# Optimization experiments

Hardware: AMD Instinct MI355X
Metric: run time of the kernel (lower is better)

Reference implementation:

```python
import jax, jax.numpy as jnp
import numpy as np
from jax import lax

DIM = 256
KS = 7
EPS = 1e-6


def setup_inputs() -> dict:
    key = jax.random.key(0)
    ks = jax.random.split(key, 10)
    x = jax.random.normal(ks[0], (32, DIM, 56, 56), dtype=jnp.float32)
    mask = jax.random.randint(ks[1], (32, 1, 7, 7), 0, 2, dtype=jnp.int32)
    dw_w = jax.random.normal(ks[2], (DIM, 1, KS, KS), dtype=jnp.float32) * (1.0 / KS)
    dw_b = jax.random.normal(ks[3], (DIM,), dtype=jnp.float32) * 0.01
    ln_w = jnp.ones((DIM,), dtype=jnp.float32)
    ln_b = jnp.zeros((DIM,), dtype=jnp.float32)
    w1 = jax.random.normal(ks[4], (DIM, 4 * DIM), dtype=jnp.float32) * (1.0 / np.sqrt(DIM))
    b1 = jax.random.normal(ks[5], (4 * DIM,), dtype=jnp.float32) * 0.01
    w2 = jax.random.normal(ks[6], (4 * DIM, DIM), dtype=jnp.float32) * (1.0 / np.sqrt(4 * DIM))
    b2 = jax.random.normal(ks[7], (DIM,), dtype=jnp.float32) * 0.01
    gamma = jnp.full((DIM,), 1e-6, dtype=jnp.float32)
    return {"x": x, "mask": mask, "dw_w": dw_w, "dw_b": dw_b, "ln_w": ln_w,
            "ln_b": ln_b, "w1": w1, "b1": b1, "w2": w2, "b2": b2, "gamma": gamma}


def _expand_mask(mask, H, W):
    # repeat_interleave the (B,1,f,f) mask up to (B,1,H,W)
    hr, wr = H // mask.shape[-2], W // mask.shape[-1]
    m = jnp.repeat(jnp.repeat(mask, hr, axis=2), wr, axis=3)
    return m


def reference(x, mask, dw_w, dw_b, ln_w, ln_b, w1, b1, w2, b2, gamma):
    B, C, H, W = x.shape
    m = _expand_mask(mask, H, W).astype(x.dtype)  # (B,1,H,W)
    inp = x
    # depthwise conv, 'same' padding
    pad = KS // 2
    y = lax.conv_general_dilated(
        x, dw_w, window_strides=(1, 1), padding=[(pad, pad), (pad, pad)],
        feature_group_count=C, dimension_numbers=("NCHW", "OIHW", "NCHW"))
    y = y + dw_b[None, :, None, None]
    y = y.transpose(0, 2, 3, 1)  # (B,H,W,C)
    # sparse LayerNorm: gather-norm-scatter == per-position LN zeroed at inactive
    mu = jnp.mean(y, axis=-1, keepdims=True)
    var = jnp.mean((y - mu) ** 2, axis=-1, keepdims=True)
    y = ((y - mu) * lax.rsqrt(var + EPS)) * ln_w + ln_b
    y = y * m[:, 0, :, :, None]
    # MLP
    h = jax.nn.gelu(jnp.einsum("bhwc,cd->bhwd", y, w1) + b1, approximate=False)
    z = (jnp.einsum("bhwd,dc->bhwc", h, w2) + b2) * gamma
    z = z.transpose(0, 3, 1, 2)  # (B,C,H,W)
    z = z * m
    return inp + z
```

## Files before the change

### kernel.cpp

```cpp
#include <hip/hip_runtime.h>
#include <math.h>

#define HW   56
#define DIMC 256
#define HID  1024

typedef __attribute__((ext_vector_type(8))) short bf16x8;
typedef __attribute__((ext_vector_type(4))) float f32x4;

__device__ __forceinline__ short f2bf(float f) {
  union { float fv; unsigned u; } v; v.fv = f;
  unsigned r = v.u + 0x7fffu + ((v.u >> 16) & 1u);
  return (short)(r >> 16);
}
__device__ __forceinline__ float bf2f(short s) {
  union { unsigned u; float fv; } v; v.u = ((unsigned)(unsigned short)s) << 16;
  return v.fv;
}
__device__ __forceinline__ float gelu_fast(float v) {
  float e = exp2f(-2.4556260f * v);
  return v * __builtin_amdgcn_rcpf(1.f + e);
}
__device__ __forceinline__ long pk8(float f0, float f1, float f2, float f3,
                                    float f4, float f5, float f6, float f7) {
  int lo = __builtin_amdgcn_cvt_pk_fp8_f32(f0, f1, 0, false);
  lo = __builtin_amdgcn_cvt_pk_fp8_f32(f2, f3, lo, true);
  int hi = __builtin_amdgcn_cvt_pk_fp8_f32(f4, f5, 0, false);
  hi = __builtin_amdgcn_cvt_pk_fp8_f32(f6, f7, hi, true);
  return ((long)(unsigned)lo) | ((long)hi << 32);
}
__device__ __forceinline__ char f2fp8(float f) {
  return (char)(__builtin_amdgcn_cvt_pk_fp8_f32(f, f, 0, false) & 0xff);
}

__global__ void prep_pack(const float* __restrict__ w1, const float* __restrict__ w2,
                          long* __restrict__ w1p, long* __restrict__ w2p,
                          int* __restrict__ qmeta) {
  int g = blockIdx.x * 256 + threadIdx.x;
  if (g == 0) { qmeta[0] = 0; qmeta[1] = 0; qmeta[2] = 0; }
  int f = g >> 6, lane = g & 63;
  int l15 = lane & 15, q = lane >> 4;
  float t[8];
  if (f < 512) {
    int k8 = f & 7, tt = f >> 3, nt = tt & 1, ch = tt >> 1;
    int n = ch * 32 + nt * 16 + l15;
    int k = k8 * 32 + q * 8;
    #pragma unroll
    for (int j = 0; j < 8; ++j) t[j] = w1[(k + j) * HID + n];
    w1p[f * 64 + lane] = pk8(t[0], t[1], t[2], t[3], t[4], t[5], t[6], t[7]);
  } else {
    int f2 = f - 512;
    int nt2 = f2 & 15, ch = f2 >> 4;
    int k = ch * 32 + q * 8;
    int c = nt2 * 16 + l15;
    #pragma unroll
    for (int j = 0; j < 8; ++j) t[j] = w2[(k + j) * DIMC + c];
    w2p[f2 * 64 + lane] = pk8(t[0], t[1], t[2], t[3], t[4], t[5], t[6], t[7]);
  }
}

__global__ void compact_k(const int* __restrict__ mask, int* __restrict__ qmeta) {
  int t = blockIdx.x * 256 + threadIdx.x;
  if (t < 1568 && mask[t]) {
    int i = atomicAdd(qmeta, 1);
    qmeta[16 + i] = t;
  }
}

__global__ __launch_bounds__(256, 4) void conv_k(
    const float* __restrict__ x, const int* __restrict__ mask,
    const float* __restrict__ dw_w, const float* __restrict__ dw_b,
    short* __restrict__ ybuf) {
  __shared__ __align__(16) float s_plane[62 * 64];
  __shared__ __align__(16) short s_out[56 * 64];

  int bid = blockIdx.x;
  int c = bid & 255, b = bid >> 8;
  int tid = threadIdx.x;
  const float* xp = x + (long)(b * DIMC + c) * HW * HW;

  #pragma unroll
  for (int it = 0; it < 4; ++it) {
    int slot = tid + 256 * it;
    if (slot < 992) {
      int row = slot >> 4, jj = slot & 15;
      f32x4 v = (f32x4){0.f, 0.f, 0.f, 0.f};
      if (row >= 3 && row < 59 && jj >= 1 && jj <= 14)
        v = *(const f32x4*)(xp + (row - 3) * HW + (jj * 4 - 4));
      *(f32x4*)(s_plane + row * 64 + jj * 4) = v;
    }
  }

  float wt[49];
  #pragma unroll
  for (int j = 0; j < 49; ++j) {
    int wi = __builtin_amdgcn_readfirstlane(__builtin_bit_cast(int, dw_w[c * 49 + j]));
    wt[j] = __builtin_bit_cast(float, wi);
  }
  float db = dw_b[c];
  __syncthreads();

  int cp = tid & 31, rg = tid >> 5;
  if (cp < 28) {
    int col0 = cp * 2, wb = col0 >> 3;
    int r0 = rg * 7;
    int mrow = 0;
    #pragma unroll
    for (int hb = 0; hb < 7; ++hb)
      mrow |= (mask[(b * 7 + hb) * 7 + wb] ? 1 : 0) << hb;
    int hb1 = r0 >> 3, hb2 = (r0 + 6) >> 3;
    if (mrow & ((2 << hb2) - (1 << hb1))) {
      float W[7][10];
#define LDROW(S, LR) do { int _o = (LR) * 64 + col0;                         \
      W[S][0] = s_plane[_o + 0]; W[S][1] = s_plane[_o + 1];                  \
      W[S][2] = s_plane[_o + 2]; W[S][3] = s_plane[_o + 3];                  \
      W[S][4] = s_plane[_o + 4]; W[S][5] = s_plane[_o + 5];                  \
      W[S][6] = s_plane[_o + 6]; W[S][7] = s_plane[_o + 7];                  \
      W[S][8] = s_plane[_o + 8]; W[S][9] = s_plane[_o + 9]; } while (0)
      LDROW(0, r0 + 0); LDROW(1, r0 + 1); LDROW(2, r0 + 2);
      LDROW(3, r0 + 3); LDROW(4, r0 + 4); LDROW(5, r0 + 5);
      #pragma unroll
      for (int k = 0; k < 7; ++k) {
        LDROW((6 + k) % 7, r0 + 6 + k);
        int r = r0 + k;
        if ((mrow >> (r >> 3)) & 1) {
          float out0 = 0.f, out1 = 0.f;
          #pragma unroll
          for (int dy = 0; dy < 7; ++dy) {
            const float* wr = wt + dy * 7;
            const float* ww = W[(k + dy) % 7];
            #pragma unroll
            for (int dx = 0; dx < 7; ++dx) {
              out0 += wr[dx] * ww[1 + dx];
              out1 += wr[dx] * ww[2 + dx];
            }
          }
          unsigned pk = (unsigned)(unsigned short)f2bf(out0 + db)
                      | ((unsigned)(unsigned short)f2bf(out1 + db) << 16);
          ((int*)s_out)[r * 32 + cp] = (int)pk;
        }
      }
#undef LDROW
    }
  }
  __syncthreads();

  #pragma unroll
  for (int it = 0; it < 2; ++it) {
    int u = tid + 256 * it;
    if (u < 392) {
      int hh = u & 7, th = u >> 3;
      int hbL = th / 7, wbL = th % 7;
      int tile = (b * 7 + hbL) * 7 + wbL;
      if (mask[tile]) {
        bf16x8 v = *(const bf16x8*)(s_out + (hbL * 8 + hh) * 64 + wbL * 8);
        *(bf16x8*)(ybuf + ((long)tile * DIMC + c) * 64 + hh * 8) = v;
      }
    }
  }
}

__global__ __launch_bounds__(256, 3) void mlp_k(
    const float* __restrict__ ln_w, const float* __restrict__ ln_b,
    const float* __restrict__ b1v, const float* __restrict__ b2v,
    const float* __restrict__ gammav,
    const long* __restrict__ w1p, const long* __restrict__ w2p,
    int* __restrict__ qmeta, short* __restrict__ ybuf) {
  __shared__ __align__(16) char smem[46592];
  __shared__ int s_u;
  short* s_a   = (short*)smem;
  short* s_del = (short*)smem;
  char*  s_h8  = smem + 36864;
  float* s_p1  = (float*)(smem + 41984);
  float* s_p2  = (float*)(smem + 43008);
  float* s_mu  = (float*)(smem + 44032);
  float* s_rs  = (float*)(smem + 44288);
  float* s_lnw = (float*)(smem + 44544);
  float* s_lnb = (float*)(smem + 45568);

  const int* list = qmeta + 16;
  int tid = threadIdx.x;
  int total = qmeta[0];

  s_lnw[tid] = ln_w[tid];
  s_lnb[tid] = ln_b[tid];

  const int wv = tid >> 6, lane = tid & 63;
  const int l15 = lane & 15, q = lane >> 4;
  const int mh = wv & 1, nh = wv >> 1;

  for (;;) {
    if (tid == 0) s_u = atomicAdd(qmeta + 1, 1);
    __syncthreads();
    int i = s_u;
    if (i >= total) break;
    int tile = list[i];
    short* ytile = ybuf + (long)tile * DIMC * 64;

    #pragma unroll
    for (int k = 0; k < 8; ++k) {
      int q4 = tid + 256 * k;
      int c = q4 & 255, pd = (q4 >> 8) * 8;
      bf16x8 v = *(const bf16x8*)(ytile + c * 64 + pd);
      #pragma unroll
      for (int j = 0; j < 8; ++j) s_a[(pd + j) * 264 + c] = v[j];
    }
    __syncthreads();

    {
      int p = tid & 63, cq = tid >> 6;
      bf16x8 va[8];
      float s1 = 0.f, s2 = 0.f;
      #pragma unroll
      for (int ii = 0; ii < 8; ++ii) {
        va[ii] = *(const bf16x8*)(s_a + p * 264 + cq * 64 + ii * 8);
        #pragma unroll
        for (int j = 0; j < 8; ++j) {
          float f = bf2f(va[ii][j]);
          s1 += f; s2 += f * f;
        }
      }
      s_p1[cq * 64 + p] = s1; s_p2[cq * 64 + p] = s2;
      __syncthreads();
      if (tid < 64) {
        float t1 = s_p1[tid] + s_p1[64 + tid] + s_p1[128 + tid] + s_p1[192 + tid];
        float t2 = s_p2[tid] + s_p2[64 + tid] + s_p2[128 + tid] + s_p2[192 + tid];
        float mu = t1 * (1.f / 256.f);
        float var = t2 * (1.f / 256.f) - mu * mu;
        s_mu[tid] = mu; s_rs[tid] = rsqrtf(var + 1e-6f);
      }
      __syncthreads();
      float mu = s_mu[p], rs = s_rs[p];
      #pragma unroll
      for (int ii = 0; ii < 8; ++ii) {
        int c0 = cq * 64 + ii * 8;
        bf16x8 v = va[ii];
        #pragma unroll
        for (int j = 0; j < 8; ++j)
          v[j] = f2bf((bf2f(v[j]) - mu) * rs * s_lnw[c0 + j] + s_lnb[c0 + j]);
        *(bf16x8*)(s_a + p * 264 + c0) = v;
      }
    }
    __syncthreads();

    const short* aRow0 = s_a + (32 * mh + l15) * 264 + q * 8;
    const short* aRow1 = s_a + (32 * mh + 16 + l15) * 264 + q * 8;
    long a0f[8], a1f[8];
    #pragma unroll
    for (int k8 = 0; k8 < 8; ++k8) {
      bf16x8 v0 = *(const bf16x8*)(aRow0 + k8 * 32);
      bf16x8 v1 = *(const bf16x8*)(aRow1 + k8 * 32);
      a0f[k8] = pk8(bf2f(v0[0]), bf2f(v0[1]), bf2f(v0[2]), bf2f(v0[3]),
                    bf2f(v0[4]), bf2f(v0[5]), bf2f(v0[6]), bf2f(v0[7]));
      a1f[k8] = pk8(bf2f(v1[0]), bf2f(v1[1]), bf2f(v1[2]), bf2f(v1[3]),
                    bf2f(v1[4]), bf2f(v1[5]), bf2f(v1[6]), bf2f(v1[7]));
    }

    f32x4 z[4][4];
    #pragma unroll
    for (int jt = 0; jt < 4; ++jt)
      #pragma unroll
      for (int Mt = 0; Mt < 4; ++Mt) z[jt][Mt] = (f32x4){0.f, 0.f, 0.f, 0.f};

    long w1r[8];
    #pragma unroll
    for (int k8 = 0; k8 < 8; ++k8)
      w1r[k8] = w1p[(long)(nh * 8 + k8) * 64 + lane];

    for (int ch = 0; ch < 32; ++ch) {
      long w2r[4];
      #pragma unroll
      for (int jt = 0; jt < 4; ++jt)
        w2r[jt] = w2p[(long)(ch * 16 + wv * 4 + jt) * 64 + lane];
      float bb = b1v[ch * 32 + 16 * nh + l15];

      f32x4 acc0 = (f32x4){0.f, 0.f, 0.f, 0.f};
      f32x4 acc1 = (f32x4){0.f, 0.f, 0.f, 0.f};
      __builtin_amdgcn_s_setprio(1);
      #pragma unroll
      for (int k8 = 0; k8 < 8; ++k8) {
        acc0 = __builtin_amdgcn_mfma_f32_16x16x32_fp8_fp8(a0f[k8], w1r[k8], acc0, 0, 0, 0);
        acc1 = __builtin_amdgcn_mfma_f32_16x16x32_fp8_fp8(a1f[k8], w1r[k8], acc1, 0, 0, 0);
      }
      __builtin_amdgcn_s_setprio(0);
      long w1n[8];
      if (ch < 31) {
        #pragma unroll
        for (int k8 = 0; k8 < 8; ++k8)
          w1n[k8] = w1p[(long)(((ch + 1) * 2 + nh) * 8 + k8) * 64 + lane];
      }
      char* hb = s_h8 + (ch & 1) * 2560;
      #pragma unroll
      for (int r = 0; r < 4; ++r) {
        hb[(32 * mh + 4 * q + r) * 40 + 16 * nh + l15]      = f2fp8(gelu_fast(acc0[r] + bb));
        hb[(32 * mh + 16 + 4 * q + r) * 40 + 16 * nh + l15] = f2fp8(gelu_fast(acc1[r] + bb));
      }
      __syncthreads();
      __builtin_amdgcn_s_setprio(1);
      #pragma unroll
      for (int Mt = 0; Mt < 4; ++Mt) {
        long aH = *(const long*)(hb + (16 * Mt + l15) * 40 + q * 8);
        #pragma unroll
        for (int jt = 0; jt < 4; ++jt)
          z[jt][Mt] = __builtin_amdgcn_mfma_f32_16x16x32_fp8_fp8(aH, w2r[jt], z[jt][Mt], 0, 0, 0);
      }
      __builtin_amdgcn_s_setprio(0);
      if (ch < 31) {
        #pragma unroll
        for (int k8 = 0; k8 < 8; ++k8) w1r[k8] = w1n[k8];
      }
    }

    #pragma unroll
    for (int jt = 0; jt < 4; ++jt) {
      int c = wv * 64 + jt * 16 + l15;
      float bb = b2v[c], gm = gammav[c];
      #pragma unroll
      for (int Mt = 0; Mt < 4; ++Mt) {
        #pragma unroll
        for (int r = 0; r < 4; ++r)
          s_del[c * 72 + 16 * Mt + 4 * q + r] = f2bf((z[jt][Mt][r] + bb) * gm);
      }
    }
    __syncthreads();
    #pragma unroll
    for (int k = 0; k < 8; ++k) {
      int q4 = tid + 256 * k;
      int c = q4 & 255, pd = (q4 >> 8) * 8;
      bf16x8 v = *(const bf16x8*)(s_del + c * 72 + pd);
      *(bf16x8*)(ytile + c * 64 + pd) = v;
    }
    __syncthreads();
  }
}

__global__ __launch_bounds__(256) void epi_k(
    const float* __restrict__ x, const int* __restrict__ mask,
    const short* __restrict__ delta, float* __restrict__ out) {
  const int NU = 32 * DIMC * HW * 7;
  int stride = gridDim.x * 256;
  for (int u = blockIdx.x * 256 + threadIdx.x; u < NU; u += stride) {
    int wb = u % 7; int t1 = u / 7;
    int h = t1 % 56; int t2 = t1 / 56;
    int c = t2 & 255; int b = t2 >> 8;
    int g = ((b * DIMC + c) * HW + h) * HW + wb * 8;
    f32x4 x0 = *(const f32x4*)(x + g);
    f32x4 x1 = *(const f32x4*)(x + g + 4);
    int tile = (b * 7 + (h >> 3)) * 7 + wb;
    if (mask[tile]) {
      bf16x8 d = *(const bf16x8*)(delta + ((long)tile * DIMC + c) * 64 + (h & 7) * 8);
      #pragma unroll
      for (int i = 0; i < 4; ++i) { x0[i] += bf2f(d[i]); x1[i] += bf2f(d[4 + i]); }
    }
    *(f32x4*)(out + g) = x0;
    *(f32x4*)(out + g + 4) = x1;
  }
}

extern "C" void kernel_launch(void* const* d_in, const int* in_sizes, int n_in,
                              void* d_out, int out_size, void* d_ws, size_t ws_size,
                              hipStream_t stream) {
  const float* x    = (const float*)d_in[0];
  const int*   mask = (const int*)d_in[1];
  const float* dw_w = (const float*)d_in[2];
  const float* dw_b = (const float*)d_in[3];
  const float* ln_w = (const float*)d_in[4];
  const float* ln_b = (const float*)d_in[5];
  const float* w1   = (const float*)d_in[6];
  const float* b1   = (const float*)d_in[7];
  const float* w2   = (const float*)d_in[8];
  const float* b2   = (const float*)d_in[9];
  const float* gm   = (const float*)d_in[10];
  float* out = (float*)d_out;

  long* w1p  = (long*)d_ws;
  long* w2p  = w1p + 512 * 64;
  int*  qmeta = (int*)(w2p + 512 * 64);
  short* ybuf = (short*)((char*)qmeta + 8192);

  prep_pack<<<256, 256, 0, stream>>>(w1, w2, w1p, w2p, qmeta);
  compact_k<<<7, 256, 0, stream>>>(mask, qmeta);
  conv_k<<<8192, 256, 0, stream>>>(x, mask, dw_w, dw_b, ybuf);
  mlp_k<<<768, 256, 0, stream>>>(ln_w, ln_b, b1, b2, gm, w1p, w2p, qmeta, ybuf);
  epi_k<<<4096, 256, 0, stream>>>(x, mask, ybuf, out);
}
```

Before: 350.2 us.

## Restructure MLP kernel to 2-wave blocks with per-wave rows and fp8 delta output

The MLP kernel moves to 128-thread blocks in which each wave owns 32 token rows and all 256 output channels. This removes the inter-wave barrier between the GELU and second-GEMM stages, because each wave writes and reads its own private hidden buffer. LayerNorm is done in four 16-row phases and writes fp8 activations straight to shared memory. The delta is stored as unscaled fp8, with gamma applied in the epilogue, which halves delta traffic but gives coarser precision on the residual update. W1/W2 fragments are now reloaded from global memory by every wave on each chunk with no prefetch, raising weight load traffic and register pressure from 32 accumulator tiles.

```diff
diff --git a/kernel.cpp b/kernel.cpp
--- a/kernel.cpp
+++ b/kernel.cpp
@@ -160,34 +160,34 @@
   }
 }
 
-__global__ __launch_bounds__(256, 3) void mlp_k(
+__global__ __launch_bounds__(128, 2) void mlp_k(
     const float* __restrict__ ln_w, const float* __restrict__ ln_b,
     const float* __restrict__ b1v, const float* __restrict__ b2v,
-    const float* __restrict__ gammav,
     const long* __restrict__ w1p, const long* __restrict__ w2p,
     int* __restrict__ qmeta, short* __restrict__ ybuf) {
-  __shared__ __align__(16) char smem[46592];
+  __shared__ __align__(16) char smem[39424];
   __shared__ int s_u;
-  short* s_a   = (short*)smem;
-  short* s_del = (short*)smem;
-  char*  s_h8  = smem + 36864;
-  float* s_p1  = (float*)(smem + 41984);
-  float* s_p2  = (float*)(smem + 43008);
-  float* s_mu  = (float*)(smem + 44032);
-  float* s_rs  = (float*)(smem + 44288);
-  float* s_lnw = (float*)(smem + 44544);
-  float* s_lnb = (float*)(smem + 45568);
+  short* s_sc  = (short*)smem;
+  char*  s_del = smem;
+  char*  s_h   = smem + 16384;
+  char*  s_a8  = smem + 18944;
+  float* s_p1  = (float*)(smem + 35840);
+  float* s_p2  = (float*)(smem + 36352);
+  float* s_mu  = (float*)(smem + 36864);
+  float* s_rs  = (float*)(smem + 37120);
+  float* s_lnw = (float*)(smem + 37376);
+  float* s_lnb = (float*)(smem + 38400);
 
   const int* list = qmeta + 16;
   int tid = threadIdx.x;
   int total = qmeta[0];
 
-  s_lnw[tid] = ln_w[tid];
-  s_lnb[tid] = ln_b[tid];
+  s_lnw[tid] = ln_w[tid];       s_lnb[tid] = ln_b[tid];
+  s_lnw[tid + 128] = ln_w[tid + 128]; s_lnb[tid + 128] = ln_b[tid + 128];
 
   const int wv = tid >> 6, lane = tid & 63;
   const int l15 = lane & 15, q = lane >> 4;
-  const int mh = wv & 1, nh = wv >> 1;
+  const int r0 = wv * 32;
 
   for (;;) {
     if (tid == 0) s_u = atomicAdd(qmeta + 1, 1);
@@ -195,148 +195,131 @@
     int i = s_u;
     if (i >= total) break;
     int tile = list[i];
-    short* ytile = ybuf + (long)tile * DIMC * 64;
-
-    #pragma unroll
-    for (int k = 0; k < 8; ++k) {
-      int q4 = tid + 256 * k;
-      int c = q4 & 255, pd = (q4 >> 8) * 8;
-      bf16x8 v = *(const bf16x8*)(ytile + c * 64 + pd);
-      #pragma unroll
-      for (int j = 0; j < 8; ++j) s_a[(pd + j) * 264 + c] = v[j];
-    }
-    __syncthreads();
-
-    {
-      int p = tid & 63, cq = tid >> 6;
-      bf16x8 va[8];
+    const short* ytile = ybuf + (long)tile * DIMC * 64;
+
+    for (int ph = 0; ph < 4; ++ph) {
+      #pragma unroll
+      for (int it = 0; it < 4; ++it) {
+        int slot = tid + 128 * it;
+        int c = slot & 255, pd = slot >> 8;
+        bf16x8 v = *(const bf16x8*)(ytile + c * 64 + ph * 16 + pd * 8);
+        #pragma unroll
+        for (int j = 0; j < 8; ++j) s_sc[(pd * 8 + j) * 264 + c] = v[j];
+      }
+      __syncthreads();
+      int p = tid & 15, cq = tid >> 4;
+      bf16x8 va[4];
       float s1 = 0.f, s2 = 0.f;
       #pragma unroll
-      for (int ii = 0; ii < 8; ++ii) {
-        va[ii] = *(const bf16x8*)(s_a + p * 264 + cq * 64 + ii * 8);
-        #pragma unroll
-        for (int j = 0; j < 8; ++j) {
-          float f = bf2f(va[ii][j]);
-          s1 += f; s2 += f * f;
-        }
-      }
-      s_p1[cq * 64 + p] = s1; s_p2[cq * 64 + p] = s2;
+      for (int ii = 0; ii < 4; ++ii) {
+        va[ii] = *(const bf16x8*)(s_sc + p * 264 + cq * 32 + ii * 8);
+        #pragma unroll
+        for (int j = 0; j < 8; ++j) { float f = bf2f(va[ii][j]); s1 += f; s2 += f * f; }
+      }
+      s_p1[cq * 16 + p] = s1; s_p2[cq * 16 + p] = s2;
       __syncthreads();
-      if (tid < 64) {
-        float t1 = s_p1[tid] + s_p1[64 + tid] + s_p1[128 + tid] + s_p1[192 + tid];
-        float t2 = s_p2[tid] + s_p2[64 + tid] + s_p2[128 + tid] + s_p2[192 + tid];
+      if (tid < 16) {
+        float t1 = 0.f, t2 = 0.f;
+        #pragma unroll
+        for (int cqq = 0; cqq < 8; ++cqq) { t1 += s_p1[cqq * 16 + tid]; t2 += s_p2[cqq * 16 + tid]; }
         float mu = t1 * (1.f / 256.f);
         float var = t2 * (1.f / 256.f) - mu * mu;
-        s_mu[tid] = mu; s_rs[tid] = rsqrtf(var + 1e-6f);
+        s_mu[ph * 16 + tid] = mu; s_rs[ph * 16 + tid] = rsqrtf(var + 1e-6f);
       }
       __syncthreads();
-      float mu = s_mu[p], rs = s_rs[p];
-      #pragma unroll
-      for (int ii = 0; ii < 8; ++ii) {
-        int c0 = cq * 64 + ii * 8;
-        bf16x8 v = va[ii];
+      float mu = s_mu[ph * 16 + p], rs = s_rs[ph * 16 + p];
+      #pragma unroll
+      for (int ii = 0; ii < 4; ++ii) {
+        int c0 = cq * 32 + ii * 8;
+        float f[8];
         #pragma unroll
         for (int j = 0; j < 8; ++j)
-          v[j] = f2bf((bf2f(v[j]) - mu) * rs * s_lnw[c0 + j] + s_lnb[c0 + j]);
-        *(bf16x8*)(s_a + p * 264 + c0) = v;
+          f[j] = (bf2f(va[ii][j]) - mu) * rs * s_lnw[c0 + j] + s_lnb[c0 + j];
+        *(long*)(s_a8 + (ph * 16 + p) * 264 + c0) = pk8(f[0], f[1], f[2], f[3], f[4], f[5], f[6], f[7]);
       }
     }
     __syncthreads();
 
-    const short* aRow0 = s_a + (32 * mh + l15) * 264 + q * 8;
-    const short* aRow1 = s_a + (32 * mh + 16 + l15) * 264 + q * 8;
-    long a0f[8], a1f[8];
-    #pragma unroll
-    for (int k8 = 0; k8 < 8; ++k8) {
-      bf16x8 v0 = *(const bf16x8*)(aRow0 + k8 * 32);
-      bf16x8 v1 = *(const bf16x8*)(aRow1 + k8 * 32);
-      a0f[k8] = pk8(bf2f(v0[0]), bf2f(v0[1]), bf2f(v0[2]), bf2f(v0[3]),
-                    bf2f(v0[4]), bf2f(v0[5]), bf2f(v0[6]), bf2f(v0[7]));
-      a1f[k8] = pk8(bf2f(v1[0]), bf2f(v1[1]), bf2f(v1[2]), bf2f(v1[3]),
-                    bf2f(v1[4]), bf2f(v1[5]), bf2f(v1[6]), bf2f(v1[7]));
-    }
-
-    f32x4 z[4][4];
-    #pragma unroll
-    for (int jt = 0; jt < 4; ++jt)
-      #pragma unroll
-      for (int Mt = 0; Mt < 4; ++Mt) z[jt][Mt] = (f32x4){0.f, 0.f, 0.f, 0.f};
-
-    long w1r[8];
-    #pragma unroll
-    for (int k8 = 0; k8 < 8; ++k8)
-      w1r[k8] = w1p[(long)(nh * 8 + k8) * 64 + lane];
+    const char* aB0 = s_a8 + (r0 + l15) * 264 + q * 8;
+    const char* aB1 = aB0 + 16 * 264;
+    char* hw = s_h + wv * 1280;
+
+    f32x4 z[2][16];
+    #pragma unroll
+    for (int mf = 0; mf < 2; ++mf)
+      #pragma unroll
+      for (int cf = 0; cf < 16; ++cf) z[mf][cf] = (f32x4){0.f, 0.f, 0.f, 0.f};
 
     for (int ch = 0; ch < 32; ++ch) {
-      long w2r[4];
-      #pragma unroll
-      for (int jt = 0; jt < 4; ++jt)
-        w2r[jt] = w2p[(long)(ch * 16 + wv * 4 + jt) * 64 + lane];
-      float bb = b1v[ch * 32 + 16 * nh + l15];
-
-      f32x4 acc0 = (f32x4){0.f, 0.f, 0.f, 0.f};
-      f32x4 acc1 = (f32x4){0.f, 0.f, 0.f, 0.f};
+      long w1f0[8], w1f1[8], w2f[16];
+      #pragma unroll
+      for (int k8 = 0; k8 < 8; ++k8) {
+        w1f0[k8] = w1p[(long)((ch * 2 + 0) * 8 + k8) * 64 + lane];
+        w1f1[k8] = w1p[(long)((ch * 2 + 1) * 8 + k8) * 64 + lane];
+      }
+      #pragma unroll
+      for (int cf = 0; cf < 16; ++cf)
+        w2f[cf] = w2p[(long)(ch * 16 + cf) * 64 + lane];
+      float bb0 = b1v[ch * 32 + l15];
+      float bb1 = b1v[ch * 32 + 16 + l15];
+
+      f32x4 a00 = (f32x4){0.f,0.f,0.f,0.f}, a01 = (f32x4){0.f,0.f,0.f,0.f};
+      f32x4 a10 = (f32x4){0.f,0.f,0.f,0.f}, a11 = (f32x4){0.f,0.f,0.f,0.f};
       __builtin_amdgcn_s_setprio(1);
       #pragma unroll
       for (int k8 = 0; k8 < 8; ++k8) {
-        acc0 = __builtin_amdgcn_mfma_f32_16x16x32_fp8_fp8(a0f[k8], w1r[k8], acc0, 0, 0, 0);
-        acc1 = __builtin_amdgcn_mfma_f32_16x16x32_fp8_fp8(a1f[k8], w1r[k8], acc1, 0, 0, 0);
+        long a0 = *(const long*)(aB0 + k8 * 32);
+        long a1 = *(const long*)(aB1 + k8 * 32);
+        a00 = __builtin_amdgcn_mfma_f32_16x16x32_fp8_fp8(a0, w1f0[k8], a00, 0, 0, 0);
+        a01 = __builtin_amdgcn_mfma_f32_16x16x32_fp8_fp8(a0, w1f1[k8], a01, 0, 0, 0);
+        a10 = __builtin_amdgcn_mfma_f32_16x16x32_fp8_fp8(a1, w1f0[k8], a10, 0, 0, 0);
+        a11 = __builtin_amdgcn_mfma_f32_16x16x32_fp8_fp8(a1, w1f1[k8], a11, 0, 0, 0);
       }
       __builtin_amdgcn_s_setprio(0);
-      long w1n[8];
-      if (ch < 31) {
-        #pragma unroll
-        for (int k8 = 0; k8 < 8; ++k8)
-          w1n[k8] = w1p[(long)(((ch + 1) * 2 + nh) * 8 + k8) * 64 + lane];
-      }
-      char* hb = s_h8 + (ch & 1) * 2560;
       #pragma unroll
       for (int r = 0; r < 4; ++r) {
-        hb[(32 * mh + 4 * q + r) * 40 + 16 * nh + l15]      = f2fp8(gelu_fast(acc0[r] + bb));
-        hb[(32 * mh + 16 + 4 * q + r) * 40 + 16 * nh + l15] = f2fp8(gelu_fast(acc1[r] + bb));
-      }
-      __syncthreads();
+        hw[(q * 4 + r) * 40 + l15]           = f2fp8(gelu_fast(a00[r] + bb0));
+        hw[(q * 4 + r) * 40 + 16 + l15]      = f2fp8(gelu_fast(a01[r] + bb1));
+        hw[(16 + q * 4 + r) * 40 + l15]      = f2fp8(gelu_fast(a10[r] + bb0));
+        hw[(16 + q * 4 + r) * 40 + 16 + l15] = f2fp8(gelu_fast(a11[r] + bb1));
+      }
+      long aH0 = *(const long*)(hw + l15 * 40 + q * 8);
+      long aH1 = *(const long*)(hw + (16 + l15) * 40 + q * 8);
       __builtin_amdgcn_s_setprio(1);
       #pragma unroll
-      for (int Mt = 0; Mt < 4; ++Mt) {
-        long aH = *(const long*)(hb + (16 * Mt + l15) * 40 + q * 8);
-        #pragma unroll
-        for (int jt = 0; jt < 4; ++jt)
-          z[jt][Mt] = __builtin_amdgcn_mfma_f32_16x16x32_fp8_fp8(aH, w2r[jt], z[jt][Mt], 0, 0, 0);
+      for (int cf = 0; cf < 16; ++cf) {
+        z[0][cf] = __builtin_amdgcn_mfma_f32_16x16x32_fp8_fp8(aH0, w2f[cf], z[0][cf], 0, 0, 0);
+        z[1][cf] = __builtin_amdgcn_mfma_f32_16x16x32_fp8_fp8(aH1, w2f[cf], z[1][cf], 0, 0, 0);
       }
       __builtin_amdgcn_s_setprio(0);
-      if (ch < 31) {
-        #pragma unroll
-        for (int k8 = 0; k8 < 8; ++k8) w1r[k8] = w1n[k8];
-      }
-    }
-
-    #pragma unroll
-    for (int jt = 0; jt < 4; ++jt) {
-      int c = wv * 64 + jt * 16 + l15;
-      float bb = b2v[c], gm = gammav[c];
-      #pragma unroll
-      for (int Mt = 0; Mt < 4; ++Mt) {
+    }
+
+    char* sd = s_del + wv * 8192;
+    #pragma unroll
+    for (int cf = 0; cf < 16; ++cf) {
+      int c = cf * 16 + l15;
+      float bb = b2v[c];
+      #pragma unroll
+      for (int mf = 0; mf < 2; ++mf)
         #pragma unroll
         for (int r = 0; r < 4; ++r)
-          s_del[c * 72 + 16 * Mt + 4 * q + r] = f2bf((z[jt][Mt][r] + bb) * gm);
-      }
-    }
-    __syncthreads();
-    #pragma unroll
-    for (int k = 0; k < 8; ++k) {
-      int q4 = tid + 256 * k;
-      int c = q4 & 255, pd = (q4 >> 8) * 8;
-      bf16x8 v = *(const bf16x8*)(s_del + c * 72 + pd);
-      *(bf16x8*)(ytile + c * 64 + pd) = v;
-    }
-    __syncthreads();
+          sd[c * 32 + mf * 16 + q * 4 + r] = f2fp8(z[mf][cf][r] + bb);
+    }
+    char* dtile8 = (char*)(ybuf + (long)tile * DIMC * 64);
+    #pragma unroll
+    for (int it = 0; it < 16; ++it) {
+      int u = lane + 64 * it;
+      int c = u >> 2, pd = (u & 3) * 8;
+      *(long*)(dtile8 + c * 64 + r0 + pd) = *(const long*)(sd + c * 32 + pd);
+    }
   }
 }
 
 __global__ __launch_bounds__(256) void epi_k(
     const float* __restrict__ x, const int* __restrict__ mask,
-    const short* __restrict__ delta, float* __restrict__ out) {
+    const short* __restrict__ delta, const float* __restrict__ gammav,
+    float* __restrict__ out) {
+  const char* delta8 = (const char*)delta;
   const int NU = 32 * DIMC * HW * 7;
   int stride = gridDim.x * 256;
   for (int u = blockIdx.x * 256 + threadIdx.x; u < NU; u += stride) {
@@ -348,9 +331,17 @@
     f32x4 x1 = *(const f32x4*)(x + g + 4);
     int tile = (b * 7 + (h >> 3)) * 7 + wb;
     if (mask[tile]) {
-      bf16x8 d = *(const bf16x8*)(delta + ((long)tile * DIMC + c) * 64 + (h & 7) * 8);
-      #pragma unroll
-      for (int i = 0; i < 4; ++i) { x0[i] += bf2f(d[i]); x1[i] += bf2f(d[4 + i]); }
+      long dl = *(const long*)(delta8 + (long)tile * 32768 + c * 64 + (h & 7) * 8);
+      int lo = (int)(unsigned)dl, hi = (int)((unsigned long)dl >> 32);
+      float gm = gammav[c];
+      x0[0] += gm * __builtin_amdgcn_cvt_f32_fp8(lo, 0);
+      x0[1] += gm * __builtin_amdgcn_cvt_f32_fp8(lo, 1);
+      x0[2] += gm * __builtin_amdgcn_cvt_f32_fp8(lo, 2);
+      x0[3] += gm * __builtin_amdgcn_cvt_f32_fp8(lo, 3);
+      x1[0] += gm * __builtin_amdgcn_cvt_f32_fp8(hi, 0);
+      x1[1] += gm * __builtin_amdgcn_cvt_f32_fp8(hi, 1);
+      x1[2] += gm * __builtin_amdgcn_cvt_f32_fp8(hi, 2);
+      x1[3] += gm * __builtin_amdgcn_cvt_f32_fp8(hi, 3);
     }
     *(f32x4*)(out + g) = x0;
     *(f32x4*)(out + g + 4) = x1;
@@ -381,6 +372,6 @@
   prep_pack<<<256, 256, 0, stream>>>(w1, w2, w1p, w2p, qmeta);
   compact_k<<<7, 256, 0, stream>>>(mask, qmeta);
   conv_k<<<8192, 256, 0, stream>>>(x, mask, dw_w, dw_b, ybuf);
-  mlp_k<<<768, 256, 0, stream>>>(ln_w, ln_b, b1, b2, gm, w1p, w2p, qmeta, ybuf);
-  epi_k<<<4096, 256, 0, stream>>>(x, mask, ybuf, out);
-}
+  mlp_k<<<1024, 128, 0, stream>>>(ln_w, ln_b, b1, b2, w1p, w2p, qmeta, ybuf);
+  epi_k<<<4096, 256, 0, stream>>>(x, mask, ybuf, gm, out);
+}
```

Measured after the change: 387.2 us. +10.6%, slower.

## Process eight channels per conv block with double-buffered register-prefetched planes

Applied to the files above, without the earlier changes.

Each conv block now handles 8 channels of one image instead of one, and loops over them. The next channel's plane is loaded into registers while the current channel is computed, then written into an alternate LDS buffer. This is meant to hide global-load latency and amortise per-block setup such as mask reads. In exchange the grid drops to 1024 blocks, LDS use roughly doubles, and each channel iteration adds a barrier, which may reduce occupancy and parallelism.

```diff
diff --git a/kernel.cpp b/kernel.cpp
--- a/kernel.cpp
+++ b/kernel.cpp
@@ -71,59 +71,83 @@
     const float* __restrict__ x, const int* __restrict__ mask,
     const float* __restrict__ dw_w, const float* __restrict__ dw_b,
     short* __restrict__ ybuf) {
-  __shared__ __align__(16) float s_plane[62 * 64];
+  __shared__ __align__(16) float s_plane[2][62 * 64];
   __shared__ __align__(16) short s_out[56 * 64];
 
+  int tid = threadIdx.x;
   int bid = blockIdx.x;
-  int c = bid & 255, b = bid >> 8;
-  int tid = threadIdx.x;
-  const float* xp = x + (long)(b * DIMC + c) * HW * HW;
-
+  int b = bid >> 5;
+  int c0 = (bid & 31) * 8;
+
+  int srow[4], sjj[4]; bool sv[4], sok[4];
   #pragma unroll
   for (int it = 0; it < 4; ++it) {
     int slot = tid + 256 * it;
-    if (slot < 992) {
-      int row = slot >> 4, jj = slot & 15;
-      f32x4 v = (f32x4){0.f, 0.f, 0.f, 0.f};
-      if (row >= 3 && row < 59 && jj >= 1 && jj <= 14)
-        v = *(const f32x4*)(xp + (row - 3) * HW + (jj * 4 - 4));
-      *(f32x4*)(s_plane + row * 64 + jj * 4) = v;
-    }
-  }
-
-  float wt[49];
-  #pragma unroll
-  for (int j = 0; j < 49; ++j) {
-    int wi = __builtin_amdgcn_readfirstlane(__builtin_bit_cast(int, dw_w[c * 49 + j]));
-    wt[j] = __builtin_bit_cast(float, wi);
-  }
-  float db = dw_b[c];
-  __syncthreads();
+    srow[it] = slot >> 4; sjj[it] = slot & 15;
+    sv[it] = slot < 992;
+    sok[it] = sv[it] && (srow[it] >= 3) && (srow[it] < 59) && (sjj[it] >= 1) && (sjj[it] <= 14);
+  }
 
   int cp = tid & 31, rg = tid >> 5;
+  int col0 = cp * 2, wb = col0 >> 3, r0 = rg * 7;
+  int mrow = 0;
   if (cp < 28) {
-    int col0 = cp * 2, wb = col0 >> 3;
-    int r0 = rg * 7;
-    int mrow = 0;
     #pragma unroll
     for (int hb = 0; hb < 7; ++hb)
       mrow |= (mask[(b * 7 + hb) * 7 + wb] ? 1 : 0) << hb;
-    int hb1 = r0 >> 3, hb2 = (r0 + 6) >> 3;
-    if (mrow & ((2 << hb2) - (1 << hb1))) {
+  }
+  int hb1 = r0 >> 3, hb2 = (r0 + 6) >> 3;
+  bool anyrow = (cp < 28) && (mrow & ((2 << hb2) - (1 << hb1)));
+
+#define LOADP(CC, R) do {                                                     \
+    const float* _xp = x + (long)(b * DIMC + (CC)) * HW * HW;                 \
+    _Pragma("unroll")                                                         \
+    for (int _it = 0; _it < 4; ++_it) {                                       \
+      f32x4 _v = (f32x4){0.f, 0.f, 0.f, 0.f};                                 \
+      if (sok[_it])                                                           \
+        _v = *(const f32x4*)(_xp + (srow[_it] - 3) * HW + (sjj[_it] * 4 - 4));\
+      (R)[_it] = _v;                                                          \
+    } } while (0)
+#define WRITEP(BUF, R) do {                                                   \
+    _Pragma("unroll")                                                         \
+    for (int _it = 0; _it < 4; ++_it)                                         \
+      if (sv[_it])                                                            \
+        *(f32x4*)(&s_plane[BUF][srow[_it] * 64 + sjj[_it] * 4]) = (R)[_it];   \
+    } while (0)
+
+  f32x4 r[4];
+  LOADP(c0, r);
+  WRITEP(0, r);
+  LOADP(c0 + 1, r);
+  __syncthreads();
+
+  for (int pi = 0; pi < 8; ++pi) {
+    int c = c0 + pi;
+    const float* sp = &s_plane[pi & 1][0];
+
+    float wt[49];
+    #pragma unroll
+    for (int j = 0; j < 49; ++j) {
+      int wi = __builtin_amdgcn_readfirstlane(__builtin_bit_cast(int, dw_w[c * 49 + j]));
+      wt[j] = __builtin_bit_cast(float, wi);
+    }
+    float db = dw_b[c];
+
+    if (anyrow) {
       float W[7][10];
-#define LDROW(S, LR) do { int _o = (LR) * 64 + col0;                         \
-      W[S][0] = s_plane[_o + 0]; W[S][1] = s_plane[_o + 1];                  \
-      W[S][2] = s_plane[_o + 2]; W[S][3] = s_plane[_o + 3];                  \
-      W[S][4] = s_plane[_o + 4]; W[S][5] = s_plane[_o + 5];                  \
-      W[S][6] = s_plane[_o + 6]; W[S][7] = s_plane[_o + 7];                  \
-      W[S][8] = s_plane[_o + 8]; W[S][9] = s_plane[_o + 9]; } while (0)
+#define LDROW(S, LR) do { int _o = (LR) * 64 + col0;                          \
+      W[S][0] = sp[_o + 0]; W[S][1] = sp[_o + 1];                             \
+      W[S][2] = sp[_o + 2]; W[S][3] = sp[_o + 3];                             \
+      W[S][4] = sp[_o + 4]; W[S][5] = sp[_o + 5];                             \
+      W[S][6] = sp[_o + 6]; W[S][7] = sp[_o + 7];                             \
+      W[S][8] = sp[_o + 8]; W[S][9] = sp[_o + 9]; } while (0)
       LDROW(0, r0 + 0); LDROW(1, r0 + 1); LDROW(2, r0 + 2);
       LDROW(3, r0 + 3); LDROW(4, r0 + 4); LDROW(5, r0 + 5);
       #pragma unroll
       for (int k = 0; k < 7; ++k) {
         LDROW((6 + k) % 7, r0 + 6 + k);
-        int r = r0 + k;
-        if ((mrow >> (r >> 3)) & 1) {
+        int rr = r0 + k;
+        if ((mrow >> (rr >> 3)) & 1) {
           float out0 = 0.f, out1 = 0.f;
           #pragma unroll
           for (int dy = 0; dy < 7; ++dy) {
@@ -137,27 +161,34 @@
           }
           unsigned pk = (unsigned)(unsigned short)f2bf(out0 + db)
                       | ((unsigned)(unsigned short)f2bf(out1 + db) << 16);
-          ((int*)s_out)[r * 32 + cp] = (int)pk;
+          ((int*)s_out)[rr * 32 + cp] = (int)pk;
         }
       }
 #undef LDROW
     }
-  }
-  __syncthreads();
-
-  #pragma unroll
-  for (int it = 0; it < 2; ++it) {
-    int u = tid + 256 * it;
-    if (u < 392) {
-      int hh = u & 7, th = u >> 3;
-      int hbL = th / 7, wbL = th % 7;
-      int tile = (b * 7 + hbL) * 7 + wbL;
-      if (mask[tile]) {
-        bf16x8 v = *(const bf16x8*)(s_out + (hbL * 8 + hh) * 64 + wbL * 8);
-        *(bf16x8*)(ybuf + ((long)tile * DIMC + c) * 64 + hh * 8) = v;
-      }
-    }
-  }
+    __syncthreads();
+
+    #pragma unroll
+    for (int it = 0; it < 2; ++it) {
+      int u = tid + 256 * it;
+      if (u < 392) {
+        int hh = u & 7, th = u >> 3;
+        int hbL = th / 7, wbL = th % 7;
+        int tile = (b * 7 + hbL) * 7 + wbL;
+        if (mask[tile]) {
+          bf16x8 v = *(const bf16x8*)(s_out + (hbL * 8 + hh) * 64 + wbL * 8);
+          *(bf16x8*)(ybuf + ((long)tile * DIMC + c) * 64 + hh * 8) = v;
+        }
+      }
+    }
+    if (pi < 7) {
+      WRITEP((pi + 1) & 1, r);
+      if (pi < 6) LOADP(c0 + pi + 2, r);
+    }
+    __syncthreads();
+  }
+#undef LOADP
+#undef WRITEP
 }
 
 __global__ __launch_bounds__(256, 3) void mlp_k(
@@ -380,7 +411,7 @@
 
   prep_pack<<<256, 256, 0, stream>>>(w1, w2, w1p, w2p, qmeta);
   compact_k<<<7, 256, 0, stream>>>(mask, qmeta);
-  conv_k<<<8192, 256, 0, stream>>>(x, mask, dw_w, dw_b, ybuf);
+  conv_k<<<1024, 256, 0, stream>>>(x, mask, dw_w, dw_b, ybuf);
   mlp_k<<<768, 256, 0, stream>>>(ln_w, ln_b, b1, b2, gm, w1p, w2p, qmeta, ybuf);
   epi_k<<<4096, 256, 0, stream>>>(x, mask, ybuf, out);
 }
```

Result: slower. 411.5 us (+17.5%).

## Use 4x4 register-tiled depthwise conv with padded LDS; fold mask compaction into prep

Applied to the files above, without the earlier changes.

Replaces the depthwise conv work split, which used 2 outputs per thread over 7 rows, with 4x4 output tiles per thread. Each thread reads 12-float rows from LDS as vector loads and reuses them across the 4 output rows, which cuts LDS traffic per output. The LDS row stride is padded from 64 to 68 floats to reduce bank conflicts, and the skip check is now done per 8x8 mask tile. The separate mask compaction kernel is merged into an extra block of prep_pack, removing one launch. Only 196 of 256 threads do conv work, and each needs more registers for its accumulators.

```diff
diff --git a/kernel.cpp b/kernel.cpp
--- a/kernel.cpp
+++ b/kernel.cpp
@@ -34,10 +34,20 @@
 }
 
 __global__ void prep_pack(const float* __restrict__ w1, const float* __restrict__ w2,
+                          const int* __restrict__ mask,
                           long* __restrict__ w1p, long* __restrict__ w2p,
                           int* __restrict__ qmeta) {
+  if (blockIdx.x == 256) {
+    if (threadIdx.x == 0) { qmeta[0] = 0; qmeta[1] = 0; qmeta[2] = 0; }
+    __syncthreads();
+    for (int t = threadIdx.x; t < 1568; t += 256)
+      if (mask[t]) {
+        int i = atomicAdd(qmeta, 1);
+        qmeta[16 + i] = t;
+      }
+    return;
+  }
   int g = blockIdx.x * 256 + threadIdx.x;
-  if (g == 0) { qmeta[0] = 0; qmeta[1] = 0; qmeta[2] = 0; }
   int f = g >> 6, lane = g & 63;
   int l15 = lane & 15, q = lane >> 4;
   float t[8];
@@ -59,19 +69,11 @@
   }
 }
 
-__global__ void compact_k(const int* __restrict__ mask, int* __restrict__ qmeta) {
-  int t = blockIdx.x * 256 + threadIdx.x;
-  if (t < 1568 && mask[t]) {
-    int i = atomicAdd(qmeta, 1);
-    qmeta[16 + i] = t;
-  }
-}
-
 __global__ __launch_bounds__(256, 4) void conv_k(
     const float* __restrict__ x, const int* __restrict__ mask,
     const float* __restrict__ dw_w, const float* __restrict__ dw_b,
     short* __restrict__ ybuf) {
-  __shared__ __align__(16) float s_plane[62 * 64];
+  __shared__ __align__(16) float s_plane[62 * 68];
   __shared__ __align__(16) short s_out[56 * 64];
 
   int bid = blockIdx.x;
@@ -80,14 +82,14 @@
   const float* xp = x + (long)(b * DIMC + c) * HW * HW;
 
   #pragma unroll
-  for (int it = 0; it < 4; ++it) {
+  for (int it = 0; it < 5; ++it) {
     int slot = tid + 256 * it;
-    if (slot < 992) {
-      int row = slot >> 4, jj = slot & 15;
+    if (slot < 1054) {
+      int row = slot / 17, jj = slot - row * 17;
       f32x4 v = (f32x4){0.f, 0.f, 0.f, 0.f};
       if (row >= 3 && row < 59 && jj >= 1 && jj <= 14)
         v = *(const f32x4*)(xp + (row - 3) * HW + (jj * 4 - 4));
-      *(f32x4*)(s_plane + row * 64 + jj * 4) = v;
+      *(f32x4*)(s_plane + row * 68 + jj * 4) = v;
     }
   }
 
@@ -100,47 +102,47 @@
   float db = dw_b[c];
   __syncthreads();
 
-  int cp = tid & 31, rg = tid >> 5;
-  if (cp < 28) {
-    int col0 = cp * 2, wb = col0 >> 3;
-    int r0 = rg * 7;
-    int mrow = 0;
-    #pragma unroll
-    for (int hb = 0; hb < 7; ++hb)
-      mrow |= (mask[(b * 7 + hb) * 7 + wb] ? 1 : 0) << hb;
-    int hb1 = r0 >> 3, hb2 = (r0 + 6) >> 3;
-    if (mrow & ((2 << hb2) - (1 << hb1))) {
-      float W[7][10];
-#define LDROW(S, LR) do { int _o = (LR) * 64 + col0;                         \
-      W[S][0] = s_plane[_o + 0]; W[S][1] = s_plane[_o + 1];                  \
-      W[S][2] = s_plane[_o + 2]; W[S][3] = s_plane[_o + 3];                  \
-      W[S][4] = s_plane[_o + 4]; W[S][5] = s_plane[_o + 5];                  \
-      W[S][6] = s_plane[_o + 6]; W[S][7] = s_plane[_o + 7];                  \
-      W[S][8] = s_plane[_o + 8]; W[S][9] = s_plane[_o + 9]; } while (0)
-      LDROW(0, r0 + 0); LDROW(1, r0 + 1); LDROW(2, r0 + 2);
-      LDROW(3, r0 + 3); LDROW(4, r0 + 4); LDROW(5, r0 + 5);
-      #pragma unroll
-      for (int k = 0; k < 7; ++k) {
-        LDROW((6 + k) % 7, r0 + 6 + k);
-        int r = r0 + k;
-        if ((mrow >> (r >> 3)) & 1) {
-          float out0 = 0.f, out1 = 0.f;
-          #pragma unroll
-          for (int dy = 0; dy < 7; ++dy) {
-            const float* wr = wt + dy * 7;
-            const float* ww = W[(k + dy) % 7];
+  if (tid < 196) {
+    int cg = tid % 14, rq = tid / 14;
+    int tile = (b * 7 + (rq >> 1)) * 7 + (cg >> 1);
+    if (mask[tile]) {
+      int R0 = rq * 4, C0 = cg * 4;
+      float acc[4][4];
+      #pragma unroll
+      for (int j = 0; j < 4; ++j)
+        #pragma unroll
+        for (int i = 0; i < 4; ++i) acc[j][i] = 0.f;
+
+      #pragma unroll
+      for (int ri = 0; ri < 10; ++ri) {
+        const float* base = s_plane + (R0 + ri) * 68 + C0;
+        f32x4 q0 = *(const f32x4*)(base);
+        f32x4 q1 = *(const f32x4*)(base + 4);
+        f32x4 q2 = *(const f32x4*)(base + 8);
+        float row[12] = {q0[0], q0[1], q0[2], q0[3],
+                         q1[0], q1[1], q1[2], q1[3],
+                         q2[0], q2[1], q2[2], q2[3]};
+        #pragma unroll
+        for (int j = 0; j < 4; ++j) {
+          if (ri >= j && ri <= j + 6) {
+            const float* wr = wt + (ri - j) * 7;
             #pragma unroll
-            for (int dx = 0; dx < 7; ++dx) {
-              out0 += wr[dx] * ww[1 + dx];
-              out1 += wr[dx] * ww[2 + dx];
-            }
+            for (int i = 0; i < 4; ++i)
+              #pragma unroll
+              for (int dx = 0; dx < 7; ++dx)
+                acc[j][i] += wr[dx] * row[i + dx + 1];
           }
-          unsigned pk = (unsigned)(unsigned short)f2bf(out0 + db)
-                      | ((unsigned)(unsigned short)f2bf(out1 + db) << 16);
-          ((int*)s_out)[r * 32 + cp] = (int)pk;
         }
       }
-#undef LDROW
+      #pragma unroll
+      for (int j = 0; j < 4; ++j) {
+        unsigned lo = (unsigned)(unsigned short)f2bf(acc[j][0] + db)
+                    | ((unsigned)(unsigned short)f2bf(acc[j][1] + db) << 16);
+        unsigned hi = (unsigned)(unsigned short)f2bf(acc[j][2] + db)
+                    | ((unsigned)(unsigned short)f2bf(acc[j][3] + db) << 16);
+        long pk = ((long)(unsigned)lo) | ((long)hi << 32);
+        *(long*)(s_out + (R0 + j) * 64 + C0) = pk;
+      }
     }
   }
   __syncthreads();
@@ -378,8 +380,7 @@
   int*  qmeta = (int*)(w2p + 512 * 64);
   short* ybuf = (short*)((char*)qmeta + 8192);
 
-  prep_pack<<<256, 256, 0, stream>>>(w1, w2, w1p, w2p, qmeta);
-  compact_k<<<7, 256, 0, stream>>>(mask, qmeta);
+  prep_pack<<<257, 256, 0, stream>>>(w1, w2, mask, w1p, w2p, qmeta);
   conv_k<<<8192, 256, 0, stream>>>(x, mask, dw_w, dw_b, ybuf);
   mlp_k<<<768, 256, 0, stream>>>(ln_w, ln_b, b1, b2, gm, w1p, w2p, qmeta, ybuf);
   epi_k<<<4096, 256, 0, stream>>>(x, mask, ybuf, out);
```

New measurement: 344.8 us. About the same (-1.6%).
